# Kernel optimization log

Hardware: AMD Instinct MI355X
Metric: run time of the kernel (lower is better)

Reference implementation:

```python
import jax, jax.numpy as jnp
import numpy as np
import math

B, N, CS = 1, 2048, 384
H, C, PQK, PV = 12, 16, 4, 8
INF, EPS = 100000.0, 1e-08


def setup_inputs() -> dict:
    key = jax.random.key(0)
    ks = jax.random.split(key, 16)
    hc = H * C
    hpq = H * PQK * 3
    hpkv = H * (PQK + PV) * 3
    cod = H * (C + 4 * PV)
    sc = 0.02
    return {
        "s": jax.random.normal(ks[0], (B, N, CS), jnp.float32),
        "rot": jax.random.normal(ks[1], (B, N, 3, 3), jnp.float32),
        "trans": jax.random.normal(ks[2], (B, N, 3), jnp.float32),
        "mask": jnp.ones((B, N), jnp.float32),
        "Wq": jax.random.normal(ks[3], (hc, CS), jnp.float32) * sc,
        "bq": jnp.zeros((hc,), jnp.float32),
        "Wkv": jax.random.normal(ks[4], (2 * hc, CS), jnp.float32) * sc,
        "bkv": jnp.zeros((2 * hc,), jnp.float32),
        "Wqp": jax.random.normal(ks[5], (hpq, CS), jnp.float32) * sc,
        "bqp": jnp.zeros((hpq,), jnp.float32),
        "Wkvp": jax.random.normal(ks[6], (hpkv, CS), jnp.float32) * sc,
        "bkvp": jnp.zeros((hpkv,), jnp.float32),
        "head_weights": jnp.full((H,), 0.541324854612918, jnp.float32),
        "Wout": jax.random.normal(ks[7], (CS, H * cod // H), jnp.float32) * sc,
        "bout": jnp.zeros((CS,), jnp.float32),
    }


def _points(s, W, b, rot, trans, npts):
    # torch.split into 3 chunks of H*npts then stack at -1 -> [B,N,H*npts,3]
    p = jnp.einsum("bni,oi->bno", s, W) + b
    p = jnp.moveaxis(p.reshape(B, N, 3, H * npts), -2, -1)  # [B,N,H*npts,3]
    p = jnp.einsum("bnij,bnmj->bnmi", rot, p) + trans[:, :, None, :]  # rigid apply
    return p.reshape(B, N, H, npts, 3)


def reference(s, rot, trans, mask, Wq, bq, Wkv, bkv, Wqp, bqp, Wkvp, bkvp, head_weights, Wout, bout):
    q = (jnp.einsum("bni,oi->bno", s, Wq) + bq).reshape(B, N, H, C)
    kv = (jnp.einsum("bni,oi->bno", s, Wkv) + bkv).reshape(B, N, H, 2 * C)
    k, v = kv[..., :C], kv[..., C:]

    q_pts = _points(s, Wqp, bqp, rot, trans, PQK)             # [B,N,H,PQK,3]
    kv_pts = _points(s, Wkvp, bkvp, rot, trans, PQK + PV)
    k_pts, v_pts = kv_pts[..., :PQK, :], kv_pts[..., PQK:, :]  # [B,N,H,PQK,3], [B,N,H,PV,3]

    a = jnp.einsum("bihc,bjhc->bhij", q, k) * math.sqrt(1.0 / (3 * C))

    # sum_{p,c} |q_pts_i - k_pts_j|^2 via norm expansion (avoids [N,N,P,3])
    q2 = jnp.moveaxis(jnp.sum(q_pts ** 2, axis=(-1, -2)), -1, 1)  # [B,H,N]
    k2 = jnp.moveaxis(jnp.sum(k_pts ** 2, axis=(-1, -2)), -1, 1)
    cross = jnp.einsum("bihpc,bjhpc->bhij", q_pts, k_pts)
    d2 = q2[..., :, None] + k2[..., None, :] - 2.0 * cross       # [B,H,N,N]

    hw = jax.nn.softplus(head_weights) * math.sqrt(1.0 / (3 * (PQK * 9.0 / 2)))
    pt_att = -0.5 * hw[None, :, None, None] * d2

    sq_mask = INF * (mask[:, None, :, None] * mask[:, None, None, :] - 1.0)  # [B,1,N,N]
    a = jax.nn.softmax(a + pt_att + sq_mask, axis=-1)

    o = jnp.einsum("bhij,bjhc->bihc", a, v).reshape(B, N, H * C)
    o_pt = jnp.einsum("bhij,bjhpc->bihpc", a, v_pts)             # [B,N,H,PV,3]
    o_pt = jnp.einsum("bnji,bnhpj->bnhpi", rot, o_pt - trans[:, :, None, None, :])  # invert_apply

    dists = jnp.sqrt(jnp.sum(o_pt ** 2, axis=-1) + EPS).reshape(B, N, H * PV)
    o_pt_f = o_pt.reshape(B, N, H * PV, 3)
    feats = jnp.concatenate([o, o_pt_f[..., 0], o_pt_f[..., 1], o_pt_f[..., 2], dists], axis=-1)
    return jnp.einsum("bnf,of->bno", feats, Wout) + bout
```

## Files before the change

### kernel.cpp

```cpp
#include <hip/hip_runtime.h>
#include <hip/hip_bf16.h>
#include <cstdint>
#include <cstddef>

#define Hh    12
#define Nseq  2048
#define PSTR  1152
#define EPSm  1e-8f
#define MASKV 1024.0f

typedef unsigned short ushort_t;
typedef __attribute__((ext_vector_type(8))) short bf8_t;
typedef __attribute__((ext_vector_type(4))) short s4_t;
typedef __attribute__((ext_vector_type(4))) float f4_t;

#define OFF_PALL   0
#define OFF_WALLB  2359296
#define OFF_BALL   2580480
#define OFF_SB     2581632
#define OFF_WOUTB  2974848
#define OFF_FEATSB 3085440
#define OFF_AU     3675264
#define OFF_KU     4068480
#define OFF_VU     4461696
#define WS_FLOATS  5051520

__device__ __forceinline__ ushort_t bfr(float x) {
    union { float f; uint32_t u; } v; v.f = x;
    uint32_t r = v.u + 0x7FFFu + ((v.u >> 16) & 1u);
    return (ushort_t)(r >> 16);
}

__global__ __launch_bounds__(256) void prep(
    const float* __restrict__ s, const float* __restrict__ Wout,
    const float* __restrict__ Wq, const float* __restrict__ Wkv,
    const float* __restrict__ Wqp, const float* __restrict__ Wkvp,
    const float* __restrict__ bq, const float* __restrict__ bkv,
    const float* __restrict__ bqp, const float* __restrict__ bkvp,
    ushort_t* __restrict__ Wallb, float* __restrict__ ball,
    ushort_t* __restrict__ sb, ushort_t* __restrict__ Woutb)
{
    int idx = blockIdx.x * 256 + threadIdx.x;
    if (idx < 1152 * 384) {
        int r = idx / 384, c = idx % 384;
        float v;
        if (r < 192)      v = Wq [(size_t)r * 384 + c];
        else if (r < 576) v = Wkv[(size_t)(r - 192) * 384 + c];
        else if (r < 720) v = Wqp[(size_t)(r - 576) * 384 + c];
        else              v = Wkvp[(size_t)(r - 720) * 384 + c];
        Wallb[idx] = bfr(v);
    }
    if (idx < 1152) {
        float v;
        if (idx < 192)      v = bq[idx];
        else if (idx < 576) v = bkv[idx - 192];
        else if (idx < 720) v = bqp[idx - 576];
        else                v = bkvp[idx - 720];
        ball[idx] = v;
    }
    if (idx < 2048 * 384) sb[idx] = bfr(s[idx]);
    if (idx < 384 * 576)  Woutb[idx] = bfr(Wout[idx]);
}

template<int BM, int BN>
__global__ __launch_bounds__(256) void gemm_mfma(
    const ushort_t* __restrict__ A, const ushort_t* __restrict__ W,
    const float* __restrict__ bias, float* __restrict__ C,
    int M, int Nn, int K)
{
    constexpr int WM = BM / 2, WN = BN / 2;
    constexpr int MI = WM / 16, NJ = WN / 16;
    __shared__ ushort_t As[BM][40];
    __shared__ ushort_t Bs[BN][40];

    const int bm = blockIdx.y * BM;
    const int bn = blockIdx.x * BN;
    const int t  = threadIdx.x;
    const int w  = t >> 6, lane = t & 63;
    const int m  = lane & 15, quad = lane >> 4;
    const int wm = (w >> 1) * WM, wn = (w & 1) * WN;

    f4_t acc[MI][NJ];
    #pragma unroll
    for (int i2 = 0; i2 < MI; ++i2)
        #pragma unroll
        for (int j2 = 0; j2 < NJ; ++j2)
            acc[i2][j2] = (f4_t){0.f, 0.f, 0.f, 0.f};

    for (int k0 = 0; k0 < K; k0 += 32) {
        #pragma unroll
        for (int u = 0; u < BM / 64; ++u) {
            int e = t + u * 256;
            int r = e >> 2, kk = (e & 3) * 8;
            *(uint4*)&As[r][kk] = *(const uint4*)&A[(size_t)(bm + r) * K + k0 + kk];
        }
        #pragma unroll
        for (int u = 0; u < BN / 64; ++u) {
            int e = t + u * 256;
            int r = e >> 2, kk = (e & 3) * 8;
            *(uint4*)&Bs[r][kk] = *(const uint4*)&W[(size_t)(bn + r) * K + k0 + kk];
        }
        __syncthreads();
        bf8_t af[MI], bf[NJ];
        #pragma unroll
        for (int x = 0; x < MI; ++x) af[x] = *(const bf8_t*)&As[wm + x * 16 + m][quad * 8];
        #pragma unroll
        for (int x = 0; x < NJ; ++x) bf[x] = *(const bf8_t*)&Bs[wn + x * 16 + m][quad * 8];
        #pragma unroll
        for (int i2 = 0; i2 < MI; ++i2)
            #pragma unroll
            for (int j2 = 0; j2 < NJ; ++j2)
                acc[i2][j2] = __builtin_amdgcn_mfma_f32_16x16x32_bf16(
                    af[i2], bf[j2], acc[i2][j2], 0, 0, 0);
        __syncthreads();
    }

    #pragma unroll
    for (int j2 = 0; j2 < NJ; ++j2) {
        int col = bn + wn + j2 * 16 + m;
        float bb = bias[col];
        #pragma unroll
        for (int i2 = 0; i2 < MI; ++i2) {
            #pragma unroll
            for (int r = 0; r < 4; ++r) {
                int row = bm + wm + i2 * 16 + quad * 4 + r;
                C[(size_t)row * Nn + col] = acc[i2][j2][r] + bb;
            }
        }
    }
}

__global__ __launch_bounds__(128) void pack_aug(
    const float* __restrict__ Pall, const float* __restrict__ rot,
    const float* __restrict__ trans, const float* __restrict__ mask,
    const float* __restrict__ hwv,
    ushort_t* __restrict__ AU, ushort_t* __restrict__ KU,
    ushort_t* __restrict__ VU)
{
    __shared__ float S[8][1156];
    const int n0 = blockIdx.x * 8;
    const int t  = threadIdx.x;

    #pragma unroll
    for (int u = 0; u < 18; ++u) {
        int f = t + u * 128;
        int rr = f / 288, c4 = f % 288;
        float4 v = *(const float4*)&Pall[(size_t)(n0 + rr) * PSTR + c4 * 4];
        *(float4*)&S[rr][c4 * 4] = v;
    }
    __syncthreads();

    if (t >= 96) return;
    const int nl = t & 7, h = t >> 3;
    const int n  = n0 + nl;
    const float* row = S[nl];

    const float whw = 0.5f * logf(1.0f + expf(hwv[h])) * 0.13608276348795434f;
    const float scale_a = 0.14433756729740643f;

    float R[9], T[3];
    #pragma unroll
    for (int z = 0; z < 9; ++z) R[z] = rot[(size_t)n * 9 + z];
    #pragma unroll
    for (int d = 0; d < 3; ++d) T[d] = trans[(size_t)n * 3 + d];

    float qpv[12], q2 = 0.f;
    #pragma unroll
    for (int p = 0; p < 4; ++p) {
        float r0 = row[576 +   0 + h * 4 + p];
        float r1 = row[576 +  48 + h * 4 + p];
        float r2 = row[576 +  96 + h * 4 + p];
        #pragma unroll
        for (int d = 0; d < 3; ++d) {
            float o = R[d*3+0]*r0 + R[d*3+1]*r1 + R[d*3+2]*r2 + T[d];
            qpv[p * 3 + d] = o;
            q2 += o * o;
        }
    }

    float kpv[12], vpv[24], k2 = 0.f;
    #pragma unroll
    for (int pt = 0; pt < 12; ++pt) {
        float r0 = row[720 +   0 + h * 12 + pt];
        float r1 = row[720 + 144 + h * 12 + pt];
        float r2 = row[720 + 288 + h * 12 + pt];
        #pragma unroll
        for (int d = 0; d < 3; ++d) {
            float o = R[d*3+0]*r0 + R[d*3+1]*r1 + R[d*3+2]*r2 + T[d];
            if (pt < 4) { kpv[pt * 3 + d] = o; k2 += o * o; }
            else        { vpv[(pt - 4) * 3 + d] = o; }
        }
    }

    const float mi = mask[n];

    __align__(16) ushort_t a32[32];
    #pragma unroll
    for (int c = 0; c < 16; ++c) a32[c] = bfr(row[h * 16 + c] * scale_a);
    #pragma unroll
    for (int z = 0; z < 12; ++z) a32[16 + z] = bfr(qpv[z] * (2.0f * whw));
    a32[28] = bfr(-whw);
    a32[29] = bfr(-whw * q2);
    a32[30] = bfr(mi * MASKV);
    a32[31] = bfr(-MASKV);
    ushort_t* adst = AU + ((size_t)h * Nseq + n) * 32;
    #pragma unroll
    for (int u = 0; u < 4; ++u) ((uint4*)adst)[u] = ((const uint4*)a32)[u];

    const float* kvrow = row + 192 + h * 32;
    __align__(16) ushort_t k32[32];
    #pragma unroll
    for (int c = 0; c < 16; ++c) k32[c] = bfr(kvrow[c]);
    #pragma unroll
    for (int z = 0; z < 12; ++z) k32[16 + z] = bfr(kpv[z]);
    k32[28] = bfr(k2);
    k32[29] = 0x3F80;
    k32[30] = bfr(mi);
    k32[31] = 0x3F80;
    ushort_t* kdst = KU + ((size_t)h * Nseq + n) * 32;
    #pragma unroll
    for (int u = 0; u < 4; ++u) ((uint4*)kdst)[u] = ((const uint4*)k32)[u];

    ushort_t* vb = VU + (size_t)h * 48 * Nseq + n;
    #pragma unroll
    for (int c = 0; c < 16; ++c) vb[(size_t)c * Nseq] = bfr(kvrow[16 + c]);
    #pragma unroll
    for (int z = 0; z < 24; ++z) vb[(size_t)(16 + z) * Nseq] = bfr(vpv[z]);
    vb[(size_t)40 * Nseq] = 0x3F80;
    #pragma unroll
    for (int c = 41; c < 48; ++c) vb[(size_t)c * Nseq] = 0;
}

__device__ __forceinline__ bf8_t expack(f4_t s) {
    s4_t p;
    p[0] = (short)bfr(__expf(s[0]));
    p[1] = (short)bfr(__expf(s[1]));
    p[2] = (short)bfr(__expf(s[2]));
    p[3] = (short)bfr(__expf(s[3]));
    s4_t z = (s4_t)0;
    return __builtin_shufflevector(p, z, 0, 1, 2, 3, 4, 5, 6, 7);
}

__device__ __forceinline__ bf8_t vpad(s4_t v) {
    s4_t z = (s4_t)0;
    return __builtin_shufflevector(v, z, 0, 1, 2, 3, 4, 5, 6, 7);
}

__global__ __launch_bounds__(256, 3) void attn_mfma(
    const ushort_t* __restrict__ AU, const ushort_t* __restrict__ KU,
    const ushort_t* __restrict__ VU,
    const float* __restrict__ rot, const float* __restrict__ trans,
    ushort_t* __restrict__ featsb)
{
    __shared__ float red[4][32][49];

    const int b    = blockIdx.x;
    const int h    = b >> 6;
    const int ib   = b & 63;
    const int t    = threadIdx.x;
    const int w    = t >> 6;
    const int lane = t & 63;
    const int m    = lane & 15;
    const int quad = lane >> 4;
    const int i0   = ib * 32;

    bf8_t afA = *(const bf8_t*)(AU + ((size_t)h * Nseq + i0 +      m) * 32 + quad * 8);
    bf8_t afB = *(const bf8_t*)(AU + ((size_t)h * Nseq + i0 + 16 + m) * 32 + quad * 8);

    f4_t acc[6];
    #pragma unroll
    for (int z = 0; z < 6; ++z) acc[z] = (f4_t){0.f, 0.f, 0.f, 0.f};

    const int jb0 = w * 512;
    const ushort_t* kb_base = KU + ((size_t)h * Nseq + jb0 + m) * 32 + quad * 8;
    const ushort_t* v_base  = VU + ((size_t)h * 48 + m) * Nseq + jb0 + quad * 4;

    for (int jt = 0; jt < 16; ++jt) {
        const int j32 = jt * 32;
        bf8_t kb0 = *(const bf8_t*)(kb_base + (size_t)j32 * 32);
        bf8_t kb1 = *(const bf8_t*)(kb_base + (size_t)(j32 + 16) * 32);
        s4_t vX0 = *(const s4_t*)(v_base + j32);
        s4_t vX1 = *(const s4_t*)(v_base + 16 * Nseq + j32);
        s4_t vX2 = *(const s4_t*)(v_base + 32 * Nseq + j32);
        s4_t vY0 = *(const s4_t*)(v_base + j32 + 16);
        s4_t vY1 = *(const s4_t*)(v_base + 16 * Nseq + j32 + 16);
        s4_t vY2 = *(const s4_t*)(v_base + 32 * Nseq + j32 + 16);

        f4_t zz = (f4_t){0.f, 0.f, 0.f, 0.f};
        f4_t sXA = __builtin_amdgcn_mfma_f32_16x16x32_bf16(kb0, afA, zz, 0, 0, 0);
        f4_t sXB = __builtin_amdgcn_mfma_f32_16x16x32_bf16(kb0, afB, zz, 0, 0, 0);
        f4_t sYA = __builtin_amdgcn_mfma_f32_16x16x32_bf16(kb1, afA, zz, 0, 0, 0);
        f4_t sYB = __builtin_amdgcn_mfma_f32_16x16x32_bf16(kb1, afB, zz, 0, 0, 0);

        bf8_t pXA = expack(sXA), pXB = expack(sXB);
        bf8_t pYA = expack(sYA), pYB = expack(sYB);
        bf8_t f0 = vpad(vX0), f1 = vpad(vX1), f2 = vpad(vX2);
        bf8_t g0 = vpad(vY0), g1 = vpad(vY1), g2 = vpad(vY2);

        acc[0] = __builtin_amdgcn_mfma_f32_16x16x32_bf16(pXA, f0, acc[0], 0, 0, 0);
        acc[0] = __builtin_amdgcn_mfma_f32_16x16x32_bf16(pYA, g0, acc[0], 0, 0, 0);
        acc[1] = __builtin_amdgcn_mfma_f32_16x16x32_bf16(pXA, f1, acc[1], 0, 0, 0);
        acc[1] = __builtin_amdgcn_mfma_f32_16x16x32_bf16(pYA, g1, acc[1], 0, 0, 0);
        acc[2] = __builtin_amdgcn_mfma_f32_16x16x32_bf16(pXA, f2, acc[2], 0, 0, 0);
        acc[2] = __builtin_amdgcn_mfma_f32_16x16x32_bf16(pYA, g2, acc[2], 0, 0, 0);
        acc[3] = __builtin_amdgcn_mfma_f32_16x16x32_bf16(pXB, f0, acc[3], 0, 0, 0);
        acc[3] = __builtin_amdgcn_mfma_f32_16x16x32_bf16(pYB, g0, acc[3], 0, 0, 0);
        acc[4] = __builtin_amdgcn_mfma_f32_16x16x32_bf16(pXB, f1, acc[4], 0, 0, 0);
        acc[4] = __builtin_amdgcn_mfma_f32_16x16x32_bf16(pYB, g1, acc[4], 0, 0, 0);
        acc[5] = __builtin_amdgcn_mfma_f32_16x16x32_bf16(pXB, f2, acc[5], 0, 0, 0);
        acc[5] = __builtin_amdgcn_mfma_f32_16x16x32_bf16(pYB, g2, acc[5], 0, 0, 0);
    }

    #pragma unroll
    for (int r = 0; r < 4; ++r) {
        red[w][quad * 4 + r][m]           = acc[0][r];
        red[w][quad * 4 + r][16 + m]      = acc[1][r];
        red[w][quad * 4 + r][32 + m]      = acc[2][r];
        red[w][16 + quad * 4 + r][m]      = acc[3][r];
        red[w][16 + quad * 4 + r][16 + m] = acc[4][r];
        red[w][16 + quad * 4 + r][32 + m] = acc[5][r];
    }
    __syncthreads();

    #pragma unroll
    for (int u = 0; u < 6; ++u) {
        int e = t + u * 256;
        int rr = e / 48, cc = e % 48;
        red[0][rr][cc] = red[0][rr][cc] + red[1][rr][cc] + red[2][rr][cc] + red[3][rr][cc];
    }
    __syncthreads();

    if (t < 32) {
        const int i = i0 + t;
        float L   = red[0][t][40];
        float inv = 1.0f / L;
        float o[40];
        #pragma unroll
        for (int z = 0; z < 40; ++z) o[z] = red[0][t][z] * inv;

        ushort_t* f = featsb + (size_t)i * 576;
        #pragma unroll
        for (int c = 0; c < 16; ++c) f[h * 16 + c] = bfr(o[c]);

        float R[9], T[3];
        #pragma unroll
        for (int z = 0; z < 9; ++z) R[z] = rot[(size_t)i * 9 + z];
        #pragma unroll
        for (int d = 0; d < 3; ++d) T[d] = trans[(size_t)i * 3 + d];

        #pragma unroll
        for (int p8 = 0; p8 < 8; ++p8) {
            float g0 = o[16 + p8 * 3 + 0] - T[0];
            float g1 = o[16 + p8 * 3 + 1] - T[1];
            float g2 = o[16 + p8 * 3 + 2] - T[2];
            float xx = R[0] * g0 + R[3] * g1 + R[6] * g2;
            float yy = R[1] * g0 + R[4] * g1 + R[7] * g2;
            float zz = R[2] * g0 + R[5] * g1 + R[8] * g2;
            float dist = sqrtf(xx * xx + yy * yy + zz * zz + EPSm);
            f[192 + h * 8 + p8] = bfr(xx);
            f[288 + h * 8 + p8] = bfr(yy);
            f[384 + h * 8 + p8] = bfr(zz);
            f[480 + h * 8 + p8] = bfr(dist);
        }
    }
}

extern "C" void kernel_launch(void* const* d_in, const int* in_sizes, int n_in,
                              void* d_out, int out_size, void* d_ws, size_t ws_size,
                              hipStream_t stream)
{
    const float* s     = (const float*)d_in[0];
    const float* rot   = (const float*)d_in[1];
    const float* trans = (const float*)d_in[2];
    const float* mask  = (const float*)d_in[3];
    const float* Wq    = (const float*)d_in[4];
    const float* bq    = (const float*)d_in[5];
    const float* Wkv   = (const float*)d_in[6];
    const float* bkv   = (const float*)d_in[7];
    const float* Wqp   = (const float*)d_in[8];
    const float* bqp   = (const float*)d_in[9];
    const float* Wkvp  = (const float*)d_in[10];
    const float* bkvp  = (const float*)d_in[11];
    const float* hwv   = (const float*)d_in[12];
    const float* Wout  = (const float*)d_in[13];
    const float* bout  = (const float*)d_in[14];
    float* out = (float*)d_out;
    float* ws  = (float*)d_ws;

    if (ws_size < (size_t)WS_FLOATS * sizeof(float)) return;

    float*    Pall   = ws + OFF_PALL;
    ushort_t* Wallb  = (ushort_t*)(ws + OFF_WALLB);
    float*    ball   = ws + OFF_BALL;
    ushort_t* sb     = (ushort_t*)(ws + OFF_SB);
    ushort_t* Woutb  = (ushort_t*)(ws + OFF_WOUTB);
    ushort_t* featsb = (ushort_t*)(ws + OFF_FEATSB);
    ushort_t* AU     = (ushort_t*)(ws + OFF_AU);
    ushort_t* KU     = (ushort_t*)(ws + OFF_KU);
    ushort_t* VU     = (ushort_t*)(ws + OFF_VU);

    prep<<<dim3(3072), 256, 0, stream>>>(s, Wout, Wq, Wkv, Wqp, Wkvp,
                                         bq, bkv, bqp, bkvp,
                                         Wallb, ball, sb, Woutb);

    gemm_mfma<128, 64><<<dim3(1152 / 64, 2048 / 128), 256, 0, stream>>>(
        sb, Wallb, ball, Pall, 2048, 1152, 384);

    pack_aug<<<dim3(256), 128, 0, stream>>>(Pall, rot, trans, mask, hwv,
                                            AU, KU, VU);

    attn_mfma<<<dim3(768), 256, 0, stream>>>(AU, KU, VU, rot, trans, featsb);

    gemm_mfma<64, 64><<<dim3(384 / 64, 2048 / 64), 256, 0, stream>>>(
        featsb, Woutb, bout, out, 2048, 384, 576);
}
```

Measured before the change: 153.0 us.

## Fuse bf16 conversion into GEMM loads and prefetch K/V tiles in attention

```diff
diff --git a/kernel.cpp b/kernel.cpp
--- a/kernel.cpp
+++ b/kernel.cpp
@@ -15,15 +15,11 @@
 typedef __attribute__((ext_vector_type(4))) float f4_t;
 
 #define OFF_PALL   0
-#define OFF_WALLB  2359296
-#define OFF_BALL   2580480
-#define OFF_SB     2581632
-#define OFF_WOUTB  2974848
-#define OFF_FEATSB 3085440
-#define OFF_AU     3675264
-#define OFF_KU     4068480
-#define OFF_VU     4461696
-#define WS_FLOATS  5051520
+#define OFF_FEATSB 2359296
+#define OFF_AU     2654208
+#define OFF_KU     3047424
+#define OFF_VU     3440640
+#define WS_FLOATS  4030464
 
 __device__ __forceinline__ ushort_t bfr(float x) {
     union { float f; uint32_t u; } v; v.f = x;
@@ -31,102 +27,149 @@
     return (ushort_t)(r >> 16);
 }
 
-__global__ __launch_bounds__(256) void prep(
-    const float* __restrict__ s, const float* __restrict__ Wout,
+__device__ __forceinline__ uint32_t pack2(float a, float b) {
+    return (uint32_t)bfr(a) | ((uint32_t)bfr(b) << 16);
+}
+
+__global__ __launch_bounds__(256) void gemm_proj(
+    const float* __restrict__ s,
     const float* __restrict__ Wq, const float* __restrict__ Wkv,
     const float* __restrict__ Wqp, const float* __restrict__ Wkvp,
     const float* __restrict__ bq, const float* __restrict__ bkv,
     const float* __restrict__ bqp, const float* __restrict__ bkvp,
-    ushort_t* __restrict__ Wallb, float* __restrict__ ball,
-    ushort_t* __restrict__ sb, ushort_t* __restrict__ Woutb)
-{
-    int idx = blockIdx.x * 256 + threadIdx.x;
-    if (idx < 1152 * 384) {
-        int r = idx / 384, c = idx % 384;
-        float v;
-        if (r < 192)      v = Wq [(size_t)r * 384 + c];
-        else if (r < 576) v = Wkv[(size_t)(r - 192) * 384 + c];
-        else if (r < 720) v = Wqp[(size_t)(r - 576) * 384 + c];
-        else              v = Wkvp[(size_t)(r - 720) * 384 + c];
-        Wallb[idx] = bfr(v);
-    }
-    if (idx < 1152) {
-        float v;
-        if (idx < 192)      v = bq[idx];
-        else if (idx < 576) v = bkv[idx - 192];
-        else if (idx < 720) v = bqp[idx - 576];
-        else                v = bkvp[idx - 720];
-        ball[idx] = v;
-    }
-    if (idx < 2048 * 384) sb[idx] = bfr(s[idx]);
-    if (idx < 384 * 576)  Woutb[idx] = bfr(Wout[idx]);
-}
-
-template<int BM, int BN>
-__global__ __launch_bounds__(256) void gemm_mfma(
-    const ushort_t* __restrict__ A, const ushort_t* __restrict__ W,
-    const float* __restrict__ bias, float* __restrict__ C,
-    int M, int Nn, int K)
-{
-    constexpr int WM = BM / 2, WN = BN / 2;
-    constexpr int MI = WM / 16, NJ = WN / 16;
-    __shared__ ushort_t As[BM][40];
-    __shared__ ushort_t Bs[BN][40];
-
-    const int bm = blockIdx.y * BM;
-    const int bn = blockIdx.x * BN;
+    float* __restrict__ C)
+{
+    __shared__ ushort_t As[128][40];
+    __shared__ ushort_t Bs[64][40];
+
+    const int bm = blockIdx.y * 128;
+    const int bn = blockIdx.x * 64;
     const int t  = threadIdx.x;
     const int w  = t >> 6, lane = t & 63;
     const int m  = lane & 15, quad = lane >> 4;
-    const int wm = (w >> 1) * WM, wn = (w & 1) * WN;
-
-    f4_t acc[MI][NJ];
-    #pragma unroll
-    for (int i2 = 0; i2 < MI; ++i2)
-        #pragma unroll
-        for (int j2 = 0; j2 < NJ; ++j2)
+    const int wm = (w >> 1) * 64, wn = (w & 1) * 32;
+
+    f4_t acc[4][2];
+    #pragma unroll
+    for (int i2 = 0; i2 < 4; ++i2)
+        #pragma unroll
+        for (int j2 = 0; j2 < 2; ++j2)
             acc[i2][j2] = (f4_t){0.f, 0.f, 0.f, 0.f};
 
-    for (int k0 = 0; k0 < K; k0 += 32) {
-        #pragma unroll
-        for (int u = 0; u < BM / 64; ++u) {
+    for (int k0 = 0; k0 < 384; k0 += 32) {
+        #pragma unroll
+        for (int u = 0; u < 4; ++u) {
             int e = t + u * 256;
-            int r = e >> 2, kk = (e & 3) * 8;
-            *(uint4*)&As[r][kk] = *(const uint4*)&A[(size_t)(bm + r) * K + k0 + kk];
-        }
-        #pragma unroll
-        for (int u = 0; u < BN / 64; ++u) {
+            int r = e >> 3, kk = (e & 7) * 4;
+            float4 va = *(const float4*)&s[(size_t)(bm + r) * 384 + k0 + kk];
+            uint2 pk; pk.x = pack2(va.x, va.y); pk.y = pack2(va.z, va.w);
+            *(uint2*)&As[r][kk] = pk;
+        }
+        #pragma unroll
+        for (int u = 0; u < 2; ++u) {
             int e = t + u * 256;
-            int r = e >> 2, kk = (e & 3) * 8;
-            *(uint4*)&Bs[r][kk] = *(const uint4*)&W[(size_t)(bn + r) * K + k0 + kk];
+            int r = e >> 3, kk = (e & 7) * 4;
+            int rr = bn + r;
+            const float* wp;
+            if (rr < 192)      wp = Wq   + (size_t)rr * 384;
+            else if (rr < 576) wp = Wkv  + (size_t)(rr - 192) * 384;
+            else if (rr < 720) wp = Wqp  + (size_t)(rr - 576) * 384;
+            else               wp = Wkvp + (size_t)(rr - 720) * 384;
+            float4 vb = *(const float4*)&wp[k0 + kk];
+            uint2 pk; pk.x = pack2(vb.x, vb.y); pk.y = pack2(vb.z, vb.w);
+            *(uint2*)&Bs[r][kk] = pk;
         }
         __syncthreads();
-        bf8_t af[MI], bf[NJ];
-        #pragma unroll
-        for (int x = 0; x < MI; ++x) af[x] = *(const bf8_t*)&As[wm + x * 16 + m][quad * 8];
-        #pragma unroll
-        for (int x = 0; x < NJ; ++x) bf[x] = *(const bf8_t*)&Bs[wn + x * 16 + m][quad * 8];
-        #pragma unroll
-        for (int i2 = 0; i2 < MI; ++i2)
+        bf8_t af[4], bfv[2];
+        #pragma unroll
+        for (int x = 0; x < 4; ++x) af[x]  = *(const bf8_t*)&As[wm + x * 16 + m][quad * 8];
+        #pragma unroll
+        for (int x = 0; x < 2; ++x) bfv[x] = *(const bf8_t*)&Bs[wn + x * 16 + m][quad * 8];
+        #pragma unroll
+        for (int i2 = 0; i2 < 4; ++i2)
             #pragma unroll
-            for (int j2 = 0; j2 < NJ; ++j2)
+            for (int j2 = 0; j2 < 2; ++j2)
                 acc[i2][j2] = __builtin_amdgcn_mfma_f32_16x16x32_bf16(
-                    af[i2], bf[j2], acc[i2][j2], 0, 0, 0);
+                    af[i2], bfv[j2], acc[i2][j2], 0, 0, 0);
         __syncthreads();
     }
 
     #pragma unroll
-    for (int j2 = 0; j2 < NJ; ++j2) {
+    for (int j2 = 0; j2 < 2; ++j2) {
         int col = bn + wn + j2 * 16 + m;
-        float bb = bias[col];
-        #pragma unroll
-        for (int i2 = 0; i2 < MI; ++i2) {
+        float bb = (col < 192) ? bq[col] : (col < 576) ? bkv[col - 192]
+                 : (col < 720) ? bqp[col - 576] : bkvp[col - 720];
+        #pragma unroll
+        for (int i2 = 0; i2 < 4; ++i2)
             #pragma unroll
             for (int r = 0; r < 4; ++r) {
                 int row = bm + wm + i2 * 16 + quad * 4 + r;
-                C[(size_t)row * Nn + col] = acc[i2][j2][r] + bb;
+                C[(size_t)row * PSTR + col] = acc[i2][j2][r] + bb;
             }
-        }
+    }
+}
+
+__global__ __launch_bounds__(256) void gemm_out(
+    const ushort_t* __restrict__ A, const float* __restrict__ Wout,
+    const float* __restrict__ bout, float* __restrict__ C)
+{
+    __shared__ ushort_t As[64][40];
+    __shared__ ushort_t Bs[64][40];
+
+    const int bm = blockIdx.y * 64;
+    const int bn = blockIdx.x * 64;
+    const int t  = threadIdx.x;
+    const int w  = t >> 6, lane = t & 63;
+    const int m  = lane & 15, quad = lane >> 4;
+    const int wm = (w >> 1) * 32, wn = (w & 1) * 32;
+
+    f4_t acc[2][2];
+    #pragma unroll
+    for (int i2 = 0; i2 < 2; ++i2)
+        #pragma unroll
+        for (int j2 = 0; j2 < 2; ++j2)
+            acc[i2][j2] = (f4_t){0.f, 0.f, 0.f, 0.f};
+
+    for (int k0 = 0; k0 < 576; k0 += 32) {
+        {
+            int r = t >> 2, kk = (t & 3) * 8;
+            *(uint4*)&As[r][kk] = *(const uint4*)&A[(size_t)(bm + r) * 576 + k0 + kk];
+        }
+        #pragma unroll
+        for (int u = 0; u < 2; ++u) {
+            int e = t + u * 256;
+            int r = e >> 3, kk = (e & 7) * 4;
+            float4 vb = *(const float4*)&Wout[(size_t)(bn + r) * 576 + k0 + kk];
+            uint2 pk; pk.x = pack2(vb.x, vb.y); pk.y = pack2(vb.z, vb.w);
+            *(uint2*)&Bs[r][kk] = pk;
+        }
+        __syncthreads();
+        bf8_t af[2], bfv[2];
+        #pragma unroll
+        for (int x = 0; x < 2; ++x) {
+            af[x]  = *(const bf8_t*)&As[wm + x * 16 + m][quad * 8];
+            bfv[x] = *(const bf8_t*)&Bs[wn + x * 16 + m][quad * 8];
+        }
+        #pragma unroll
+        for (int i2 = 0; i2 < 2; ++i2)
+            #pragma unroll
+            for (int j2 = 0; j2 < 2; ++j2)
+                acc[i2][j2] = __builtin_amdgcn_mfma_f32_16x16x32_bf16(
+                    af[i2], bfv[j2], acc[i2][j2], 0, 0, 0);
+        __syncthreads();
+    }
+
+    #pragma unroll
+    for (int j2 = 0; j2 < 2; ++j2) {
+        int col = bn + wn + j2 * 16 + m;
+        float bb = bout[col];
+        #pragma unroll
+        for (int i2 = 0; i2 < 2; ++i2)
+            #pragma unroll
+            for (int r = 0; r < 4; ++r) {
+                int row = bm + wm + i2 * 16 + quad * 4 + r;
+                C[(size_t)row * 384 + col] = acc[i2][j2][r] + bb;
+            }
     }
 }
 
@@ -244,6 +287,24 @@
 __device__ __forceinline__ bf8_t vpad(s4_t v) {
     s4_t z = (s4_t)0;
     return __builtin_shufflevector(v, z, 0, 1, 2, 3, 4, 5, 6, 7);
+}
+
+struct KVTile { bf8_t kb0, kb1; s4_t v[6]; };
+
+__device__ __forceinline__ KVTile load_tile(
+    const ushort_t* __restrict__ kb_base, const ushort_t* __restrict__ v_base,
+    int j32)
+{
+    KVTile tl;
+    tl.kb0  = *(const bf8_t*)(kb_base + (size_t)j32 * 32);
+    tl.kb1  = *(const bf8_t*)(kb_base + (size_t)(j32 + 16) * 32);
+    tl.v[0] = *(const s4_t*)(v_base + j32);
+    tl.v[1] = *(const s4_t*)(v_base + 16 * Nseq + j32);
+    tl.v[2] = *(const s4_t*)(v_base + 32 * Nseq + j32);
+    tl.v[3] = *(const s4_t*)(v_base + j32 + 16);
+    tl.v[4] = *(const s4_t*)(v_base + 16 * Nseq + j32 + 16);
+    tl.v[5] = *(const s4_t*)(v_base + 32 * Nseq + j32 + 16);
+    return tl;
 }
 
 __global__ __launch_bounds__(256, 3) void attn_mfma(
@@ -275,27 +336,23 @@
     const ushort_t* kb_base = KU + ((size_t)h * Nseq + jb0 + m) * 32 + quad * 8;
     const ushort_t* v_base  = VU + ((size_t)h * 48 + m) * Nseq + jb0 + quad * 4;
 
+    KVTile cur = load_tile(kb_base, v_base, 0);
+
+    #pragma unroll
     for (int jt = 0; jt < 16; ++jt) {
-        const int j32 = jt * 32;
-        bf8_t kb0 = *(const bf8_t*)(kb_base + (size_t)j32 * 32);
-        bf8_t kb1 = *(const bf8_t*)(kb_base + (size_t)(j32 + 16) * 32);
-        s4_t vX0 = *(const s4_t*)(v_base + j32);
-        s4_t vX1 = *(const s4_t*)(v_base + 16 * Nseq + j32);
-        s4_t vX2 = *(const s4_t*)(v_base + 32 * Nseq + j32);
-        s4_t vY0 = *(const s4_t*)(v_base + j32 + 16);
-        s4_t vY1 = *(const s4_t*)(v_base + 16 * Nseq + j32 + 16);
-        s4_t vY2 = *(const s4_t*)(v_base + 32 * Nseq + j32 + 16);
-
         f4_t zz = (f4_t){0.f, 0.f, 0.f, 0.f};
-        f4_t sXA = __builtin_amdgcn_mfma_f32_16x16x32_bf16(kb0, afA, zz, 0, 0, 0);
-        f4_t sXB = __builtin_amdgcn_mfma_f32_16x16x32_bf16(kb0, afB, zz, 0, 0, 0);
-        f4_t sYA = __builtin_amdgcn_mfma_f32_16x16x32_bf16(kb1, afA, zz, 0, 0, 0);
-        f4_t sYB = __builtin_amdgcn_mfma_f32_16x16x32_bf16(kb1, afB, zz, 0, 0, 0);
+        f4_t sXA = __builtin_amdgcn_mfma_f32_16x16x32_bf16(cur.kb0, afA, zz, 0, 0, 0);
+        f4_t sXB = __builtin_amdgcn_mfma_f32_16x16x32_bf16(cur.kb0, afB, zz, 0, 0, 0);
+        f4_t sYA = __builtin_amdgcn_mfma_f32_16x16x32_bf16(cur.kb1, afA, zz, 0, 0, 0);
+        f4_t sYB = __builtin_amdgcn_mfma_f32_16x16x32_bf16(cur.kb1, afB, zz, 0, 0, 0);
+
+        KVTile nxt;
+        if (jt < 15) nxt = load_tile(kb_base, v_base, (jt + 1) * 32);
 
         bf8_t pXA = expack(sXA), pXB = expack(sXB);
         bf8_t pYA = expack(sYA), pYB = expack(sYB);
-        bf8_t f0 = vpad(vX0), f1 = vpad(vX1), f2 = vpad(vX2);
-        bf8_t g0 = vpad(vY0), g1 = vpad(vY1), g2 = vpad(vY2);
+        bf8_t f0 = vpad(cur.v[0]), f1 = vpad(cur.v[1]), f2 = vpad(cur.v[2]);
+        bf8_t g0 = vpad(cur.v[3]), g1 = vpad(cur.v[4]), g2 = vpad(cur.v[5]);
 
         acc[0] = __builtin_amdgcn_mfma_f32_16x16x32_bf16(pXA, f0, acc[0], 0, 0, 0);
         acc[0] = __builtin_amdgcn_mfma_f32_16x16x32_bf16(pYA, g0, acc[0], 0, 0, 0);
@@ -309,6 +366,8 @@
         acc[4] = __builtin_amdgcn_mfma_f32_16x16x32_bf16(pYB, g1, acc[4], 0, 0, 0);
         acc[5] = __builtin_amdgcn_mfma_f32_16x16x32_bf16(pXB, f2, acc[5], 0, 0, 0);
         acc[5] = __builtin_amdgcn_mfma_f32_16x16x32_bf16(pYB, g2, acc[5], 0, 0, 0);
+
+        cur = nxt;
     }
 
     #pragma unroll
@@ -390,27 +449,19 @@
     if (ws_size < (size_t)WS_FLOATS * sizeof(float)) return;
 
     float*    Pall   = ws + OFF_PALL;
-    ushort_t* Wallb  = (ushort_t*)(ws + OFF_WALLB);
-    float*    ball   = ws + OFF_BALL;
-    ushort_t* sb     = (ushort_t*)(ws + OFF_SB);
-    ushort_t* Woutb  = (ushort_t*)(ws + OFF_WOUTB);
     ushort_t* featsb = (ushort_t*)(ws + OFF_FEATSB);
     ushort_t* AU     = (ushort_t*)(ws + OFF_AU);
     ushort_t* KU     = (ushort_t*)(ws + OFF_KU);
     ushort_t* VU     = (ushort_t*)(ws + OFF_VU);
 
-    prep<<<dim3(3072), 256, 0, stream>>>(s, Wout, Wq, Wkv, Wqp, Wkvp,
-                                         bq, bkv, bqp, bkvp,
-                                         Wallb, ball, sb, Woutb);
-
-    gemm_mfma<128, 64><<<dim3(1152 / 64, 2048 / 128), 256, 0, stream>>>(
-        sb, Wallb, ball, Pall, 2048, 1152, 384);
+    gemm_proj<<<dim3(1152 / 64, 2048 / 128), 256, 0, stream>>>(
+        s, Wq, Wkv, Wqp, Wkvp, bq, bkv, bqp, bkvp, Pall);
 
     pack_aug<<<dim3(256), 128, 0, stream>>>(Pall, rot, trans, mask, hwv,
                                             AU, KU, VU);
 
     attn_mfma<<<dim3(768), 256, 0, stream>>>(AU, KU, VU, rot, trans, featsb);
 
-    gemm_mfma<64, 64><<<dim3(384 / 64, 2048 / 64), 256, 0, stream>>>(
-        featsb, Woutb, bout, out, 2048, 384, 576);
-}
+    gemm_out<<<dim3(384 / 64, 2048 / 64), 256, 0, stream>>>(
+        featsb, Wout, bout, out);
+}
```

Result: slower. 182.4 us (+19.2%).

## Tile V layout per 32-key block and software-prefetch next K/V tile

Applied to the files above, without the earlier changes.

```diff
diff --git a/kernel.cpp b/kernel.cpp
--- a/kernel.cpp
+++ b/kernel.cpp
@@ -101,17 +101,17 @@
             *(uint4*)&Bs[r][kk] = *(const uint4*)&W[(size_t)(bn + r) * K + k0 + kk];
         }
         __syncthreads();
-        bf8_t af[MI], bf[NJ];
-        #pragma unroll
-        for (int x = 0; x < MI; ++x) af[x] = *(const bf8_t*)&As[wm + x * 16 + m][quad * 8];
-        #pragma unroll
-        for (int x = 0; x < NJ; ++x) bf[x] = *(const bf8_t*)&Bs[wn + x * 16 + m][quad * 8];
+        bf8_t af[MI], bfv[NJ];
+        #pragma unroll
+        for (int x = 0; x < MI; ++x) af[x]  = *(const bf8_t*)&As[wm + x * 16 + m][quad * 8];
+        #pragma unroll
+        for (int x = 0; x < NJ; ++x) bfv[x] = *(const bf8_t*)&Bs[wn + x * 16 + m][quad * 8];
         #pragma unroll
         for (int i2 = 0; i2 < MI; ++i2)
             #pragma unroll
             for (int j2 = 0; j2 < NJ; ++j2)
                 acc[i2][j2] = __builtin_amdgcn_mfma_f32_16x16x32_bf16(
-                    af[i2], bf[j2], acc[i2][j2], 0, 0, 0);
+                    af[i2], bfv[j2], acc[i2][j2], 0, 0, 0);
         __syncthreads();
     }
 
@@ -120,13 +120,12 @@
         int col = bn + wn + j2 * 16 + m;
         float bb = bias[col];
         #pragma unroll
-        for (int i2 = 0; i2 < MI; ++i2) {
+        for (int i2 = 0; i2 < MI; ++i2)
             #pragma unroll
             for (int r = 0; r < 4; ++r) {
                 int row = bm + wm + i2 * 16 + quad * 4 + r;
                 C[(size_t)row * Nn + col] = acc[i2][j2][r] + bb;
             }
-        }
     }
 }
 
@@ -221,14 +220,14 @@
     #pragma unroll
     for (int u = 0; u < 4; ++u) ((uint4*)kdst)[u] = ((const uint4*)k32)[u];
 
-    ushort_t* vb = VU + (size_t)h * 48 * Nseq + n;
-    #pragma unroll
-    for (int c = 0; c < 16; ++c) vb[(size_t)c * Nseq] = bfr(kvrow[16 + c]);
-    #pragma unroll
-    for (int z = 0; z < 24; ++z) vb[(size_t)(16 + z) * Nseq] = bfr(vpv[z]);
-    vb[(size_t)40 * Nseq] = 0x3F80;
-    #pragma unroll
-    for (int c = 41; c < 48; ++c) vb[(size_t)c * Nseq] = 0;
+    ushort_t* vb = VU + (size_t)h * 98304 + (size_t)(n >> 5) * 1536 + (n & 31);
+    #pragma unroll
+    for (int c = 0; c < 16; ++c) vb[c * 32] = bfr(kvrow[16 + c]);
+    #pragma unroll
+    for (int z = 0; z < 24; ++z) vb[(16 + z) * 32] = bfr(vpv[z]);
+    vb[40 * 32] = 0x3F80;
+    #pragma unroll
+    for (int c = 41; c < 48; ++c) vb[c * 32] = 0;
 }
 
 __device__ __forceinline__ bf8_t expack(f4_t s) {
@@ -244,6 +243,24 @@
 __device__ __forceinline__ bf8_t vpad(s4_t v) {
     s4_t z = (s4_t)0;
     return __builtin_shufflevector(v, z, 0, 1, 2, 3, 4, 5, 6, 7);
+}
+
+struct KVTile { bf8_t kb0, kb1; s4_t v[6]; };
+
+__device__ __forceinline__ KVTile load_tile(
+    const ushort_t* __restrict__ kb_base, const ushort_t* __restrict__ vt,
+    int m, int quad)
+{
+    KVTile tl;
+    tl.kb0  = *(const bf8_t*)(kb_base);
+    tl.kb1  = *(const bf8_t*)(kb_base + 16 * 32);
+    tl.v[0] = *(const s4_t*)(vt +        m * 32 +      quad * 4);
+    tl.v[1] = *(const s4_t*)(vt +  512 + m * 32 +      quad * 4);
+    tl.v[2] = *(const s4_t*)(vt + 1024 + m * 32 +      quad * 4);
+    tl.v[3] = *(const s4_t*)(vt +        m * 32 + 16 + quad * 4);
+    tl.v[4] = *(const s4_t*)(vt +  512 + m * 32 + 16 + quad * 4);
+    tl.v[5] = *(const s4_t*)(vt + 1024 + m * 32 + 16 + quad * 4);
+    return tl;
 }
 
 __global__ __launch_bounds__(256, 3) void attn_mfma(
@@ -273,29 +290,27 @@
 
     const int jb0 = w * 512;
     const ushort_t* kb_base = KU + ((size_t)h * Nseq + jb0 + m) * 32 + quad * 8;
-    const ushort_t* v_base  = VU + ((size_t)h * 48 + m) * Nseq + jb0 + quad * 4;
-
+    const ushort_t* v_base  = VU + (size_t)h * 98304 + (size_t)jb0 * 48;
+
+    KVTile cur = load_tile(kb_base, v_base, m, quad);
+
+    #pragma unroll
     for (int jt = 0; jt < 16; ++jt) {
-        const int j32 = jt * 32;
-        bf8_t kb0 = *(const bf8_t*)(kb_base + (size_t)j32 * 32);
-        bf8_t kb1 = *(const bf8_t*)(kb_base + (size_t)(j32 + 16) * 32);
-        s4_t vX0 = *(const s4_t*)(v_base + j32);
-        s4_t vX1 = *(const s4_t*)(v_base + 16 * Nseq + j32);
-        s4_t vX2 = *(const s4_t*)(v_base + 32 * Nseq + j32);
-        s4_t vY0 = *(const s4_t*)(v_base + j32 + 16);
-        s4_t vY1 = *(const s4_t*)(v_base + 16 * Nseq + j32 + 16);
-        s4_t vY2 = *(const s4_t*)(v_base + 32 * Nseq + j32 + 16);
-
         f4_t zz = (f4_t){0.f, 0.f, 0.f, 0.f};
-        f4_t sXA = __builtin_amdgcn_mfma_f32_16x16x32_bf16(kb0, afA, zz, 0, 0, 0);
-        f4_t sXB = __builtin_amdgcn_mfma_f32_16x16x32_bf16(kb0, afB, zz, 0, 0, 0);
-        f4_t sYA = __builtin_amdgcn_mfma_f32_16x16x32_bf16(kb1, afA, zz, 0, 0, 0);
-        f4_t sYB = __builtin_amdgcn_mfma_f32_16x16x32_bf16(kb1, afB, zz, 0, 0, 0);
+        f4_t sXA = __builtin_amdgcn_mfma_f32_16x16x32_bf16(cur.kb0, afA, zz, 0, 0, 0);
+        f4_t sXB = __builtin_amdgcn_mfma_f32_16x16x32_bf16(cur.kb0, afB, zz, 0, 0, 0);
+        f4_t sYA = __builtin_amdgcn_mfma_f32_16x16x32_bf16(cur.kb1, afA, zz, 0, 0, 0);
+        f4_t sYB = __builtin_amdgcn_mfma_f32_16x16x32_bf16(cur.kb1, afB, zz, 0, 0, 0);
+
+        KVTile nxt;
+        if (jt < 15)
+            nxt = load_tile(kb_base + (size_t)(jt + 1) * 32 * 32,
+                            v_base + (size_t)(jt + 1) * 1536, m, quad);
 
         bf8_t pXA = expack(sXA), pXB = expack(sXB);
         bf8_t pYA = expack(sYA), pYB = expack(sYB);
-        bf8_t f0 = vpad(vX0), f1 = vpad(vX1), f2 = vpad(vX2);
-        bf8_t g0 = vpad(vY0), g1 = vpad(vY1), g2 = vpad(vY2);
+        bf8_t f0 = vpad(cur.v[0]), f1 = vpad(cur.v[1]), f2 = vpad(cur.v[2]);
+        bf8_t g0 = vpad(cur.v[3]), g1 = vpad(cur.v[4]), g2 = vpad(cur.v[5]);
 
         acc[0] = __builtin_amdgcn_mfma_f32_16x16x32_bf16(pXA, f0, acc[0], 0, 0, 0);
         acc[0] = __builtin_amdgcn_mfma_f32_16x16x32_bf16(pYA, g0, acc[0], 0, 0, 0);
@@ -309,6 +324,8 @@
         acc[4] = __builtin_amdgcn_mfma_f32_16x16x32_bf16(pYB, g1, acc[4], 0, 0, 0);
         acc[5] = __builtin_amdgcn_mfma_f32_16x16x32_bf16(pXB, f2, acc[5], 0, 0, 0);
         acc[5] = __builtin_amdgcn_mfma_f32_16x16x32_bf16(pYB, g2, acc[5], 0, 0, 0);
+
+        cur = nxt;
     }
 
     #pragma unroll
```

After: 139.8 us. -8.6%, faster.
